# Performance work log

Hardware: AMD Instinct MI355X
Metric: run time of the kernel (lower is better)

The kernel has to match this reference:

```python
import jax, jax.numpy as jnp
import numpy as np

SIZE = (2, 2)

def setup_inputs() -> dict:
    key = jax.random.key(0)
    k1, k2 = jax.random.split(key)
    B, H, W, C = 16, 128, 128, 64
    OH, OW = H * SIZE[0], W * SIZE[1]
    updates = jax.random.normal(k1, (B, H, W, C), dtype=jnp.float32)
    argmax = jax.random.randint(k2, (B, H, W, C), 0, OH * OW * C, dtype=jnp.int32)
    return {"updates": updates, "argmax": argmax}

def reference(updates, argmax):
    # Max-unpooling: scatter pooled values into an upsampled map at argmax positions.
    B, H, W, C = updates.shape
    OH, OW = H * SIZE[0], W * SIZE[1]
    # Decode flattened argmax (TF convention: ((y*OW + x)*C + c)) -> (y, x).
    y = (argmax // (OW * C)) % OH            # [B,H,W,C]
    x = (argmax // C) % OW                   # [B,H,W,C]
    # Batch and channel indices come from position, matching the TF code
    # (channel is taken from a tiled arange, NOT argmax % C).
    b = jnp.arange(B, dtype=jnp.int32).reshape(B, 1, 1, 1)
    c = jnp.arange(C, dtype=jnp.int32).reshape(1, 1, 1, C)
    out = jnp.zeros((B, OH, OW, C), dtype=updates.dtype)
    # tf.scatter_nd sums duplicate indices -> use .add
    out = out.at[b, y, x, c].add(updates)
    return out
```

## Files before the change

### kernel.cpp

```cpp
#include <hip/hip_runtime.h>


#define C_      64
#define N_ELEM  (16 * 128 * 128 * 64)
#define NB      1024
#define ST      512
#define CHE     8192
#define NBIN    512
#define NGB     8192
#define REGION  8192

__device__ __forceinline__ unsigned int f2bf(float f) {
    unsigned int u = __float_as_uint(f);
    return (u + 0x7fffu + ((u >> 16) & 1u)) >> 16;
}

__global__ __launch_bounds__(ST) void scatter_sort_kernel(
        const float4* __restrict__ upd4, const int4* __restrict__ amx4,
        unsigned int* __restrict__ pairs, int* __restrict__ lofs) {
    __shared__ unsigned int staging[CHE];
    __shared__ int hist[NBIN], lstart[NBIN], lcur[NBIN];
    __shared__ int wsc[16];

    int t = threadIdx.x, lane = t & 63, w = t >> 6;
    int blk = blockIdx.x;
    int cc = (t & 15) << 2;

    for (int ch = 0; ch < 2; ++ch) {
        int base4 = blk * 4096 + ch * 2048;
        int4 a[4]; float4 u[4];
        #pragma unroll
        for (int q = 0; q < 4; ++q) {
            a[q] = amx4[base4 + q * ST + t];
            u[q] = upd4[base4 + q * ST + t];
        }
        int bins[16]; unsigned int prs[16];
        #pragma unroll
        for (int q = 0; q < 4; ++q) {
            bins[4*q+0] = (a[q].x >> 13) & 511;
            prs [4*q+0] = (((unsigned)(a[q].x & 0x1FC0) | cc)       << 16) | f2bf(u[q].x);
            bins[4*q+1] = (a[q].y >> 13) & 511;
            prs [4*q+1] = (((unsigned)(a[q].y & 0x1FC0) | (cc + 1)) << 16) | f2bf(u[q].y);
            bins[4*q+2] = (a[q].z >> 13) & 511;
            prs [4*q+2] = (((unsigned)(a[q].z & 0x1FC0) | (cc + 2)) << 16) | f2bf(u[q].z);
            bins[4*q+3] = (a[q].w >> 13) & 511;
            prs [4*q+3] = (((unsigned)(a[q].w & 0x1FC0) | (cc + 3)) << 16) | f2bf(u[q].w);
        }

        hist[t] = 0;
        __syncthreads();
        #pragma unroll
        for (int j = 0; j < 16; ++j) atomicAdd(&hist[bins[j]], 1);
        __syncthreads();

        int cnt = hist[t];
        int incl = cnt;
        #pragma unroll
        for (int off = 1; off < 64; off <<= 1) {
            int nv = __shfl_up(incl, off, 64);
            if (lane >= off) incl += nv;
        }
        if (lane == 63) wsc[w] = incl;
        __syncthreads();
        if (t < 8) {
            int s = 0;
            for (int j = 0; j < t; ++j) s += wsc[j];
            wsc[8 + t] = s;
        }
        __syncthreads();
        int excl = incl - cnt + wsc[8 + w];
        lstart[t] = excl;
        lcur[t]   = excl;
        lofs[(2 * blk + ch) * NBIN + t] = excl;
        __syncthreads();

        #pragma unroll
        for (int j = 0; j < 16; ++j) {
            int slot = atomicAdd(&lcur[bins[j]], 1);
            staging[slot] = prs[j];
        }
        __syncthreads();

        uint4* dst = (uint4*)(pairs + blk * 16384 + ch * CHE);
        #pragma unroll
        for (int q = 0; q < 4; ++q) {
            int k = q * ST + t;
            dst[k] = make_uint4(staging[4*k], staging[4*k+1],
                                staging[4*k+2], staging[4*k+3]);
        }
        __syncthreads();
    }
}

__global__ __launch_bounds__(ST) void gather_accum_kernel(
        const unsigned int* __restrict__ pairs, const int* __restrict__ lofs,
        float4* __restrict__ out4) {
    __shared__ float acc[REGION];
    __shared__ int segStart[128], runBase[128];
    __shared__ int w0tot, Mtot;

    int g = blockIdx.x, t = threadIdx.x;
    int b = g >> 9, bin = g & 511;

    #pragma unroll
    for (int q = 0; q < 4; ++q)
        *(float4*)&acc[(q * ST + t) * 4] = make_float4(0.f, 0.f, 0.f, 0.f);

    int cnt = 0, incl = 0;
    if (t < 128) {
        int row = (b * 128 + t) * NBIN + bin;
        int s = lofs[row];
        int e = (bin == 511) ? CHE : lofs[row + 1];
        cnt = e - s;
        segStart[t] = s;
        incl = cnt;
        int lane = t & 63;
        #pragma unroll
        for (int off = 1; off < 64; off <<= 1) {
            int nv = __shfl_up(incl, off, 64);
            if (lane >= off) incl += nv;
        }
        if (t == 63) w0tot = incl;
    }
    __syncthreads();
    if (t < 128) {
        int base = (t >= 64) ? w0tot : 0;
        runBase[t] = base + incl - cnt;
        if (t == 127) Mtot = base + incl;
    }
    __syncthreads();

    int M = Mtot;
    for (int m = t; m < M; m += ST) {
        int lo = 0;
        #pragma unroll
        for (int stp = 64; stp; stp >>= 1)
            if (lo + stp < 128 && runBase[lo + stp] <= m) lo += stp;
        int idx = ((b * 64 + (lo >> 1)) << 14) + ((lo & 1) << 13)
                  + segStart[lo] + (m - runBase[lo]);
        unsigned int p = pairs[idx];
        atomicAdd(&acc[p >> 16], __uint_as_float(p << 16));
    }
    __syncthreads();

    float4* dst = out4 + (size_t)g * (REGION / 4);
    #pragma unroll
    for (int q = 0; q < 4; ++q) {
        int k = q * ST + t;
        dst[k] = make_float4(acc[4*k], acc[4*k+1], acc[4*k+2], acc[4*k+3]);
    }
}

__global__ void zero_out_kernel(float4* __restrict__ out, int n4) {
    int stride = gridDim.x * blockDim.x;
    for (int i = blockIdx.x * blockDim.x + threadIdx.x; i < n4; i += stride)
        out[i] = make_float4(0.f, 0.f, 0.f, 0.f);
}

__global__ void unpool_atomic_kernel(const float4* __restrict__ upd4,
                                     const int4* __restrict__ amx4,
                                     float* __restrict__ out, int n4) {
    int i = blockIdx.x * blockDim.x + threadIdx.x;
    if (i >= n4) return;
    float4 u = upd4[i];
    int4   a = amx4[i];
    int e = i << 2;
    int c = e & (C_ - 1);
    int base_b = (e >> 20) << 22;
    int y, x;
    y = (a.x >> 14) & 255; x = (a.x >> 6) & 255;
    atomicAdd(&out[base_b + (y << 14) + (x << 6) + c], u.x);
    y = (a.y >> 14) & 255; x = (a.y >> 6) & 255;
    atomicAdd(&out[base_b + (y << 14) + (x << 6) + c + 1], u.y);
    y = (a.z >> 14) & 255; x = (a.z >> 6) & 255;
    atomicAdd(&out[base_b + (y << 14) + (x << 6) + c + 2], u.z);
    y = (a.w >> 14) & 255; x = (a.w >> 6) & 255;
    atomicAdd(&out[base_b + (y << 14) + (x << 6) + c + 3], u.w);
}

extern "C" void kernel_launch(void* const* d_in, const int* in_sizes, int n_in,
                              void* d_out, int out_size, void* d_ws, size_t ws_size,
                              hipStream_t stream) {
    const float* updates = (const float*)d_in[0];
    const int*   argmax  = (const int*)d_in[1];

    size_t pair_bytes = (size_t)N_ELEM * 4;
    size_t lofs_bytes = (size_t)NB * 2 * NBIN * 4;
    size_t need = pair_bytes + lofs_bytes;

    if (in_sizes[0] == N_ELEM && ws_size >= need) {
        char* ws = (char*)d_ws;
        unsigned int* pairs = (unsigned int*)ws;
        int*          lofs  = (int*)(ws + pair_bytes);

        scatter_sort_kernel<<<NB, ST, 0, stream>>>(
            (const float4*)updates, (const int4*)argmax, pairs, lofs);
        gather_accum_kernel<<<NGB, ST, 0, stream>>>(pairs, lofs, (float4*)d_out);
    } else {
        int n_out4 = out_size >> 2;
        zero_out_kernel<<<2048, 256, 0, stream>>>((float4*)d_out, n_out4);
        int n4 = in_sizes[0] >> 2;
        unpool_atomic_kernel<<<(n4 + 255) / 256, 256, 0, stream>>>(
            (const float4*)updates, (const int4*)argmax, (float*)d_out, n4);
    }
}
```

Baseline: 169.6 us.

## Pad sorted bins to even length and gather pairs with 64-bit loads

The scatter kernel now rounds each bin's count up to an even number and fills the odd slot with a zero pair. Per-chunk offsets gain a trailing end entry, so the gather kernel can read two packed entries per uint2 load and do half as many binary searches per element. The scatter kernel also issues the second chunk's global loads before processing the first chunk, to overlap load latency with the histogram work. In exchange, the workspace and the amount of data written grow slightly, and each padding entry adds a zero into acc[0].

Result: no change. 167.8 us (-1.1%).

```diff
diff --git a/kernel.cpp b/kernel.cpp
--- a/kernel.cpp
+++ b/kernel.cpp
@@ -9,6 +9,7 @@
 #define NBIN    512
 #define NGB     8192
 #define REGION  8192
+#define PADCAP  (CHE + NBIN)
 
 __device__ __forceinline__ unsigned int f2bf(float f) {
     unsigned int u = __float_as_uint(f);
@@ -18,22 +19,24 @@
 __global__ __launch_bounds__(ST) void scatter_sort_kernel(
         const float4* __restrict__ upd4, const int4* __restrict__ amx4,
         unsigned int* __restrict__ pairs, int* __restrict__ lofs) {
-    __shared__ unsigned int staging[CHE];
-    __shared__ int hist[NBIN], lstart[NBIN], lcur[NBIN];
-    __shared__ int wsc[16];
+    __shared__ unsigned int staging[PADCAP];
+    __shared__ int h[NBIN];
+    __shared__ int wsc[17];
 
     int t = threadIdx.x, lane = t & 63, w = t >> 6;
     int blk = blockIdx.x;
     int cc = (t & 15) << 2;
 
+    int base4 = blk * 4096;
+    int4 a[4]; float4 u[4];
+    #pragma unroll
+    for (int q = 0; q < 4; ++q) {
+        a[q] = amx4[base4 + q * ST + t];
+        u[q] = upd4[base4 + q * ST + t];
+    }
+
+    #pragma unroll
     for (int ch = 0; ch < 2; ++ch) {
-        int base4 = blk * 4096 + ch * 2048;
-        int4 a[4]; float4 u[4];
-        #pragma unroll
-        for (int q = 0; q < 4; ++q) {
-            a[q] = amx4[base4 + q * ST + t];
-            u[q] = upd4[base4 + q * ST + t];
-        }
         int bins[16]; unsigned int prs[16];
         #pragma unroll
         for (int q = 0; q < 4; ++q) {
@@ -46,15 +49,23 @@
             bins[4*q+3] = (a[q].w >> 13) & 511;
             prs [4*q+3] = (((unsigned)(a[q].w & 0x1FC0) | (cc + 3)) << 16) | f2bf(u[q].w);
         }
-
-        hist[t] = 0;
-        __syncthreads();
-        #pragma unroll
-        for (int j = 0; j < 16; ++j) atomicAdd(&hist[bins[j]], 1);
-        __syncthreads();
-
-        int cnt = hist[t];
-        int incl = cnt;
+        if (ch == 0) {
+            #pragma unroll
+            for (int q = 0; q < 4; ++q) {
+                a[q] = amx4[base4 + 2048 + q * ST + t];
+                u[q] = upd4[base4 + 2048 + q * ST + t];
+            }
+        }
+
+        h[t] = 0;
+        __syncthreads();
+        #pragma unroll
+        for (int j = 0; j < 16; ++j) atomicAdd(&h[bins[j]], 1);
+        __syncthreads();
+
+        int cnt = h[t];
+        int pcnt = (cnt + 1) & ~1;
+        int incl = pcnt;
         #pragma unroll
         for (int off = 1; off < 64; off <<= 1) {
             int nv = __shfl_up(incl, off, 64);
@@ -68,26 +79,30 @@
             wsc[8 + t] = s;
         }
         __syncthreads();
-        int excl = incl - cnt + wsc[8 + w];
-        lstart[t] = excl;
-        lcur[t]   = excl;
-        lofs[(2 * blk + ch) * NBIN + t] = excl;
-        __syncthreads();
-
+        int excl = incl - pcnt + wsc[8 + w];
+        h[t] = excl;
+        int row = (2 * blk + ch) * 513;
+        lofs[row + t] = excl;
+        if (t == 511) {
+            lofs[row + 512] = excl + pcnt;
+            wsc[16] = excl + pcnt;
+        }
+        __syncthreads();
+
+        if (cnt & 1) staging[excl + cnt] = 0u;
         #pragma unroll
         for (int j = 0; j < 16; ++j) {
-            int slot = atomicAdd(&lcur[bins[j]], 1);
+            int slot = atomicAdd(&h[bins[j]], 1);
             staging[slot] = prs[j];
         }
         __syncthreads();
 
-        uint4* dst = (uint4*)(pairs + blk * 16384 + ch * CHE);
-        #pragma unroll
-        for (int q = 0; q < 4; ++q) {
-            int k = q * ST + t;
+        int padM = wsc[16];
+        uint4* dst = (uint4*)(pairs + (size_t)(2 * blk + ch) * PADCAP);
+        int n4v = (padM + 3) >> 2;
+        for (int k = t; k < n4v; k += ST)
             dst[k] = make_uint4(staging[4*k], staging[4*k+1],
                                 staging[4*k+2], staging[4*k+3]);
-        }
         __syncthreads();
     }
 }
@@ -96,8 +111,9 @@
         const unsigned int* __restrict__ pairs, const int* __restrict__ lofs,
         float4* __restrict__ out4) {
     __shared__ float acc[REGION];
-    __shared__ int segStart[128], runBase[128];
-    __shared__ int w0tot, Mtot;
+    __shared__ int segS2[128];
+    __shared__ int runB2[129];
+    __shared__ int w0t;
 
     int g = blockIdx.x, t = threadIdx.x;
     int b = g >> 9, bin = g & 511;
@@ -106,40 +122,42 @@
     for (int q = 0; q < 4; ++q)
         *(float4*)&acc[(q * ST + t) * 4] = make_float4(0.f, 0.f, 0.f, 0.f);
 
-    int cnt = 0, incl = 0;
+    int cnt2 = 0, incl = 0;
     if (t < 128) {
-        int row = (b * 128 + t) * NBIN + bin;
+        int row = (b * 128 + t) * 513 + bin;
         int s = lofs[row];
-        int e = (bin == 511) ? CHE : lofs[row + 1];
-        cnt = e - s;
-        segStart[t] = s;
-        incl = cnt;
+        int e = lofs[row + 1];
+        cnt2 = (e - s) >> 1;
+        segS2[t] = s >> 1;
+        incl = cnt2;
         int lane = t & 63;
         #pragma unroll
         for (int off = 1; off < 64; off <<= 1) {
             int nv = __shfl_up(incl, off, 64);
             if (lane >= off) incl += nv;
         }
-        if (t == 63) w0tot = incl;
+        if (t == 63) w0t = incl;
     }
     __syncthreads();
     if (t < 128) {
-        int base = (t >= 64) ? w0tot : 0;
-        runBase[t] = base + incl - cnt;
-        if (t == 127) Mtot = base + incl;
+        int base = (t >= 64) ? w0t : 0;
+        runB2[t] = base + incl - cnt2;
+        if (t == 127) runB2[128] = base + incl;
     }
     __syncthreads();
 
-    int M = Mtot;
-    for (int m = t; m < M; m += ST) {
+    int M2 = runB2[128];
+    const uint2* pr2 = (const uint2*)pairs;
+    size_t bbase2 = (size_t)b * 128 * (PADCAP / 2);
+    for (int m2 = t; m2 < M2; m2 += ST) {
         int lo = 0;
         #pragma unroll
         for (int stp = 64; stp; stp >>= 1)
-            if (lo + stp < 128 && runBase[lo + stp] <= m) lo += stp;
-        int idx = ((b * 64 + (lo >> 1)) << 14) + ((lo & 1) << 13)
-                  + segStart[lo] + (m - runBase[lo]);
-        unsigned int p = pairs[idx];
-        atomicAdd(&acc[p >> 16], __uint_as_float(p << 16));
+            if (lo + stp < 128 && runB2[lo + stp] <= m2) lo += stp;
+        uint2 p = pr2[bbase2 + (size_t)lo * (PADCAP / 2)
+                      + segS2[lo] + (m2 - runB2[lo])];
+        atomicAdd(&acc[p.x >> 16], __uint_as_float(p.x << 16));
+        atomicAdd(&acc[p.y >> 16], __uint_as_float(p.y << 16));
     }
     __syncthreads();
 
@@ -184,8 +202,8 @@
     const float* updates = (const float*)d_in[0];
     const int*   argmax  = (const int*)d_in[1];
 
-    size_t pair_bytes = (size_t)N_ELEM * 4;
-    size_t lofs_bytes = (size_t)NB * 2 * NBIN * 4;
+    size_t pair_bytes = (size_t)NB * 2 * PADCAP * 4;
+    size_t lofs_bytes = (size_t)NB * 2 * 513 * 4;
     size_t need = pair_bytes + lofs_bytes;
 
     if (in_sizes[0] == N_ELEM && ws_size >= need) {
```
